# Optimization experiments

Hardware: AMD Instinct MI355X
Metric: run time of the kernel (lower is better)

## Reference

```python
import jax, jax.numpy as jnp
import numpy as np
import math

S, B, F, D, H, L, DFF, PRED = 448, 64, 8, 256, 8, 4, 256, 96
DK = D // H
EPS = 1e-5


def _pos_enc(length, d_model):
    pos = jnp.arange(length, dtype=jnp.float32)[:, None]            # [S,1]
    div = jnp.exp(jnp.arange(0, d_model, 2, dtype=jnp.float32) * (-math.log(10000.0) / d_model))
    pe = jnp.zeros((length, d_model), jnp.float32)
    pe = pe.at[:, 0::2].set(jnp.sin(pos * div))
    pe = pe.at[:, 1::2].set(jnp.cos(pos * div))
    return pe[:, None, :]                                            # [S,1,D]


def _layernorm(x, g, b):
    mu = jnp.mean(x, axis=-1, keepdims=True)
    var = jnp.mean((x - mu) ** 2, axis=-1, keepdims=True)
    return (x - mu) / jnp.sqrt(var + EPS) * g + b


def setup_inputs() -> dict:
    key = jax.random.key(0)
    ks = jax.random.split(key, 12)
    g = lambda k, shape: (jax.random.normal(k, shape) * 0.02).astype(jnp.float32)
    return {
        "src": jax.random.normal(ks[0], (S, B, F), jnp.float32),
        "w_in": g(ks[1], (F, D)), "b_in": jnp.zeros((D,), jnp.float32),
        "Wq": g(ks[2], (L, D, D)), "bq": jnp.zeros((L, D), jnp.float32),
        "Wk": g(ks[3], (L, D, D)), "bk": jnp.zeros((L, D), jnp.float32),
        "Wv": g(ks[4], (L, D, D)), "bv": jnp.zeros((L, D), jnp.float32),
        "Wo": g(ks[5], (L, D, D)), "bo": jnp.zeros((L, D), jnp.float32),
        "g1": jnp.ones((L, D), jnp.float32), "be1": jnp.zeros((L, D), jnp.float32),
        "W1": g(ks[6], (L, D, DFF)), "b1": jnp.zeros((L, DFF), jnp.float32),
        "W2": g(ks[7], (L, DFF, D)), "b2": jnp.zeros((L, D), jnp.float32),
        "g2": jnp.ones((L, D), jnp.float32), "be2": jnp.zeros((L, D), jnp.float32),
        "w_out": g(ks[8], (D, F)), "b_out": jnp.zeros((F,), jnp.float32),
    }


def reference(src, w_in, b_in, Wq, bq, Wk, bk, Wv, bv, Wo, bo,
              g1, be1, W1, b1, W2, b2, g2, be2, w_out, b_out):
    x = src @ w_in + b_in                 # [S,B,D]
    x = x + _pos_enc(S, D)

    scale = math.sqrt(DK)

    def layer(x, p):
        wq, bq_, wk, bk_, wv, bv_, wo, bo_, g1_, be1_, w1, b1_, w2, b2_, g2_, be2_ = p
        Q = (x @ wq + bq_).reshape(S, B, H, DK)
        K = (x @ wk + bk_).reshape(S, B, H, DK)
        V = (x @ wv + bv_).reshape(S, B, H, DK)
        scores = jnp.einsum("sbhd,tbhd->bhst", Q, K) / scale   # [B,H,S,S]
        attn = jax.nn.softmax(scores, axis=-1)
        ctx = jnp.einsum("bhst,tbhd->sbhd", attn, V).reshape(S, B, D)
        x = _layernorm(x + (ctx @ wo + bo_), g1_, be1_)
        ff = jax.nn.relu(x @ w1 + b1_) @ w2 + b2_
        x = _layernorm(x + ff, g2_, be2_)
        return x, None

    x, _ = jax.lax.scan(layer, x, (Wq, bq, Wk, bk, Wv, bv, Wo, bo,
                                   g1, be1, W1, b1, W2, b2, g2, be2))
    return x[-PRED:] @ w_out + b_out      # [PRED,B,F]
```

## Files before the change

### kernel.cpp

```cpp
#include <hip/hip_runtime.h>
#include <hip/hip_bf16.h>
#include <math.h>

#define S_ 448
#define B_ 64
#define F_ 8
#define D_ 256
#define H_ 8
#define DK_ 32
#define L_ 4
#define PRED_ 96
#define NT_ (S_ * B_)
#define PANEL_ (S_ * DK_)
#define VTP_ (32 * 512)
#define SCQ_ 0.25503484f

typedef unsigned short bf16_t;
using bf16x8 = __attribute__((ext_vector_type(8))) short;
using f32x4  = __attribute__((ext_vector_type(4))) float;
using f32x16 = __attribute__((ext_vector_type(16))) float;

__device__ __forceinline__ float b2f(bf16_t b) {
  return __uint_as_float(((unsigned)b) << 16);
}
__device__ __forceinline__ bf16_t f2b(float f) {
  unsigned u = __float_as_uint(f);
  u += 0x7fffu + ((u >> 16) & 1u);
  return (bf16_t)(u >> 16);
}
__device__ __forceinline__ unsigned pk2(float lo, float hi) {
  union { __hip_bfloat162 h; unsigned u; } c;
  c.h = __float22bfloat162_rn(make_float2(lo, hi));
  return c.u;
}
__device__ __forceinline__ void gload16(const bf16_t* g, char* l) {
  __builtin_amdgcn_global_load_lds(
      (const __attribute__((address_space(1))) unsigned*)g,
      (__attribute__((address_space(3))) unsigned*)l, 16, 0, 0);
}

__global__ __launch_bounds__(256) void embed_kernel(
    const float* __restrict__ src, const float* __restrict__ w_in,
    const float* __restrict__ b_in, bf16_t* __restrict__ x) {
  int n = blockIdx.x;
  int d = threadIdx.x;
  const float* srow = src + (size_t)n * F_;
  float acc = b_in[d];
#pragma unroll
  for (int f = 0; f < F_; ++f) acc += srow[f] * w_in[f * D_ + d];
  int s = n / B_;
  int i2 = d & ~1;
  float freq = __expf(-9.210340371976184f * (float)i2 / (float)D_);
  float ang = (float)s * freq;
  float pe = (d & 1) ? cosf(ang) : sinf(ang);
  x[(size_t)n * D_ + d] = f2b(acc + pe);
}

__global__ __launch_bounds__(256) void transpose_w_kernel(
    const float* __restrict__ W, bf16_t* __restrict__ Wt, float scale) {
  __shared__ float t[32][33];
  int l = blockIdx.z;
  int k0 = blockIdx.x * 32, n0 = blockIdx.y * 32;
  int x = threadIdx.x, y = threadIdx.y;
  const float* src = W + ((size_t)l * 256 + k0) * 256 + n0;
#pragma unroll
  for (int i = y; i < 32; i += 8) t[i][x] = src[(size_t)i * 256 + x];
  __syncthreads();
  bf16_t* dst = Wt + ((size_t)l * 256 + n0) * 256 + k0;
#pragma unroll
  for (int i = y; i < 32; i += 8) dst[(size_t)i * 256 + x] = f2b(t[x][i] * scale);
}

__global__ __launch_bounds__(512) void vtrans_kernel(
    const bf16_t* __restrict__ V, bf16_t* __restrict__ Vt) {
  __shared__ bf16_t t[32][456];
  int bh = blockIdx.x, tid = threadIdx.x;
  const bf16_t* Vp = V + (size_t)bh * PANEL_;
#pragma unroll
  for (int p = 0; p < 4; ++p) {
    int idx = tid + p * 512;
    if (idx < 1792) {
      int s = idx >> 2, c = idx & 3;
      uint4 v = *(const uint4*)(Vp + s * 32 + c * 8);
      unsigned w[4] = {v.x, v.y, v.z, v.w};
#pragma unroll
      for (int e = 0; e < 8; ++e) {
        bf16_t val = (bf16_t)((e & 1) ? (w[e >> 1] >> 16) : (w[e >> 1] & 0xffff));
        *(bf16_t*)((char*)&t[0][0] + (c * 8 + e) * 912 + s * 2) = val;
      }
    }
  }
  __syncthreads();
  bf16_t* Op = Vt + (size_t)bh * VTP_;
#pragma unroll
  for (int p = 0; p < 4; ++p) {
    int idx = tid + p * 512;
    int dk = idx >> 6, sl = idx & 63;
    uint4 v = {0, 0, 0, 0};
    if (sl < 56) v = *(const uint4*)((char*)&t[0][0] + dk * 912 + sl * 16);
    *(uint4*)(Op + dk * 512 + sl * 8) = v;
  }
}

template <int ALAY, int OLAY, int RELU>
__device__ __forceinline__ void gemm_body(
    const bf16_t* __restrict__ A, const bf16_t* __restrict__ Wt,
    const float* __restrict__ bias, float bscale, bf16_t* __restrict__ Y,
    int m0, int n0) {
  __shared__ bf16_t As[2][128][32];
  __shared__ bf16_t Bs[2][128][32];
  int tid = threadIdx.x, lane = tid & 63, wv = tid >> 6;
  int wr = wv >> 2, wc = wv & 3;
  int jg = lane >> 4, fr = lane & 15;
  int s_row = tid >> 2;
  int s_p = tid & 3;

  auto stage = [&](int kt, int buf) {
    int k0 = kt * 32;
    int ls = s_p ^ ((s_row >> 1) & 3);
    const bf16_t* ap;
    if (ALAY == 0) {
      ap = A + (size_t)(m0 + s_row) * 256 + k0 + ls * 8;
    } else {
      int n = m0 + s_row;
      int k = k0 + ls * 8;
      ap = A + ((size_t)(((n & 63) << 3) | (k >> 5)) * S_ + (n >> 6)) * DK_ +
           (k & 31);
    }
    const bf16_t* bp = Wt + (size_t)(n0 + s_row) * 256 + k0 + ls * 8;
    gload16(ap, (char*)As + buf * 8192 + wv * 1024);
    gload16(bp, (char*)Bs + buf * 8192 + wv * 1024);
  };

  f32x4 zero = {0.f, 0.f, 0.f, 0.f};
  f32x4 acc[4][2];
#pragma unroll
  for (int i = 0; i < 4; ++i)
#pragma unroll
    for (int j = 0; j < 2; ++j) acc[i][j] = zero;

  stage(0, 0);
  __syncthreads();

  for (int kt = 0; kt < 8; ++kt) {
    int buf = kt & 1;
    if (kt < 7) stage(kt + 1, buf ^ 1);
    bf16x8 af[4], bfr[2];
#pragma unroll
    for (int mi = 0; mi < 4; ++mi) {
      int row = wr * 64 + mi * 16 + fr;
      af[mi] = *(const bf16x8*)((const char*)&As[buf][0][0] + row * 64 +
                                ((jg ^ ((row >> 1) & 3)) << 4));
    }
#pragma unroll
    for (int ni = 0; ni < 2; ++ni) {
      int rn = wc * 32 + ni * 16 + fr;
      bfr[ni] = *(const bf16x8*)((const char*)&Bs[buf][0][0] + rn * 64 +
                                 ((jg ^ ((rn >> 1) & 3)) << 4));
    }
#pragma unroll
    for (int mi = 0; mi < 4; ++mi)
#pragma unroll
      for (int ni = 0; ni < 2; ++ni)
        acc[mi][ni] = __builtin_amdgcn_mfma_f32_16x16x32_bf16(
            af[mi], bfr[ni], acc[mi][ni], 0, 0, 0);
    __syncthreads();
  }

  char* ep0 = (char*)&As[0][0][0] + wv * 1024;
  float bcol[2];
#pragma unroll
  for (int ni = 0; ni < 2; ++ni)
    bcol[ni] = bias[n0 + wc * 32 + ni * 16 + fr] * bscale;
#pragma unroll
  for (int mi = 0; mi < 4; ++mi) {
    char* ep = ep0 + (mi & 1) * 8192;
#pragma unroll
    for (int ni = 0; ni < 2; ++ni)
#pragma unroll
      for (int r = 0; r < 4; ++r) {
        float v = acc[mi][ni][r] + bcol[ni];
        if (RELU) v = fmaxf(v, 0.f);
        int row = jg * 4 + r;
        int cb = (ni * 16 + fr) * 2;
        *(bf16_t*)(ep + row * 64 + (cb ^ (jg << 4))) = f2b(v);
      }
    int row16 = lane >> 2, c = lane & 3;
    uint4 v = *(uint4*)(ep + row16 * 64 +
                        ((c << 4) ^ (((row16 >> 2) & 3) << 4)));
    int n = m0 + wr * 64 + mi * 16 + row16;
    if (OLAY == 0) {
      *(uint4*)((char*)(Y + (size_t)n * 256 + n0 + wc * 32) + c * 16) = v;
    } else {
      int h = (n0 + wc * 32) >> 5;
      *(uint4*)((char*)(Y + ((size_t)(((n & 63) << 3) | h) * S_ + (n >> 6)) *
                                DK_) +
                c * 16) = v;
    }
  }
}

template <int OLAY>
__device__ __forceinline__ void gemm_wide_body(
    const bf16_t* __restrict__ A, const bf16_t* __restrict__ Wt,
    const float* __restrict__ bias, float bscale, bf16_t* __restrict__ Y,
    int m0) {
  __shared__ char smem[49152];
  int tid = threadIdx.x, lane = tid & 63, wv = tid >> 6;
  int wr = wv >> 2, wc = wv & 3;
  int jg = lane >> 4, fr = lane & 15;

  auto stage = [&](int kt, int buf) {
    int k0 = kt * 32;
    int row = tid >> 2, p = tid & 3;
    int ls = p ^ ((row >> 1) & 3);
    gload16(A + (size_t)(m0 + row) * 256 + k0 + ls * 8,
            smem + buf * 8192 + wv * 1024);
    int r1 = 128 + row;
    gload16(Wt + (size_t)row * 256 + k0 + ls * 8,
            smem + 16384 + buf * 16384 + wv * 1024);
    gload16(Wt + (size_t)r1 * 256 + k0 + (p ^ ((r1 >> 1) & 3)) * 8,
            smem + 16384 + buf * 16384 + 8192 + wv * 1024);
  };

  f32x4 zero = {0.f, 0.f, 0.f, 0.f};
  f32x4 acc[4][4];
#pragma unroll
  for (int i = 0; i < 4; ++i)
#pragma unroll
    for (int j = 0; j < 4; ++j) acc[i][j] = zero;

  stage(0, 0);
  __syncthreads();

  for (int kt = 0; kt < 8; ++kt) {
    int buf = kt & 1;
    if (kt < 7) stage(kt + 1, buf ^ 1);
    bf16x8 af[4], bfr[4];
#pragma unroll
    for (int mi = 0; mi < 4; ++mi) {
      int row = wr * 64 + mi * 16 + fr;
      af[mi] = *(const bf16x8*)(smem + buf * 8192 + row * 64 +
                                ((jg ^ ((row >> 1) & 3)) << 4));
    }
#pragma unroll
    for (int ni = 0; ni < 4; ++ni) {
      int rn = wc * 64 + ni * 16 + fr;
      bfr[ni] = *(const bf16x8*)(smem + 16384 + buf * 16384 + rn * 64 +
                                 ((jg ^ ((rn >> 1) & 3)) << 4));
    }
#pragma unroll
    for (int mi = 0; mi < 4; ++mi)
#pragma unroll
      for (int ni = 0; ni < 4; ++ni)
        acc[mi][ni] = __builtin_amdgcn_mfma_f32_16x16x32_bf16(
            af[mi], bfr[ni], acc[mi][ni], 0, 0, 0);
    __syncthreads();
  }

  float bcol[4];
#pragma unroll
  for (int ni = 0; ni < 4; ++ni)
    bcol[ni] = bias[wc * 64 + ni * 16 + fr] * bscale;
#pragma unroll
  for (int mi = 0; mi < 4; ++mi) {
    char* ep = smem + ((mi & 1) ? 16384 : 0) + wv * 2048;
#pragma unroll
    for (int ni = 0; ni < 4; ++ni)
#pragma unroll
      for (int r = 0; r < 4; ++r) {
        float v = acc[mi][ni][r] + bcol[ni];
        int row = jg * 4 + r;
        int cb = (ni * 16 + fr) * 2;
        *(bf16_t*)(ep + row * 128 + (cb ^ (jg << 4))) = f2b(v);
      }
    int row16 = lane >> 2;
    int n = m0 + wr * 64 + mi * 16 + row16;
#pragma unroll
    for (int ps = 0; ps < 2; ++ps) {
      int ch = (lane & 3) + ps * 4;
      uint4 v = *(uint4*)(ep + row16 * 128 +
                          ((ch * 16) ^ (((row16 >> 2) & 3) << 4)));
      if (OLAY == 0) {
        *(uint4*)((char*)(Y + (size_t)n * 256 + wc * 64) + ch * 16) = v;
      } else {
        int h = wc * 2 + (ch >> 2);
        *(uint4*)((char*)(Y + ((size_t)(((n & 63) << 3) | h) * S_ +
                               (n >> 6)) * DK_) +
                  (ch & 3) * 16) = v;
      }
    }
  }
}

__global__ __launch_bounds__(512, 2) void gemm_qkv_kernel(
    const bf16_t* __restrict__ A, const bf16_t* __restrict__ wq,
    const bf16_t* __restrict__ wk, const bf16_t* __restrict__ wvp,
    const float* __restrict__ bq, const float* __restrict__ bk,
    const float* __restrict__ bvp, bf16_t* __restrict__ yq,
    bf16_t* __restrict__ yk, bf16_t* __restrict__ yv) {
  int bid = blockIdx.x;
  int w = (bid & 7) * 84 + (bid >> 3);
  int mtx = w % 3;
  int m0 = (w / 3) * 128;
  const bf16_t* W = mtx == 0 ? wq : mtx == 1 ? wk : wvp;
  const float* bb = mtx == 0 ? bq : mtx == 1 ? bk : bvp;
  bf16_t* Y = mtx == 0 ? yq : mtx == 1 ? yk : yv;
  float bscale = mtx == 0 ? SCQ_ : 1.0f;
  gemm_wide_body<1>(A, W, bb, bscale, Y, m0);
}

__global__ __launch_bounds__(512, 4) void gemm_relu_kernel(
    const bf16_t* __restrict__ A, const bf16_t* __restrict__ Wt,
    const float* __restrict__ bias, bf16_t* __restrict__ Y) {
  int bid = blockIdx.x;
  int w = (bid & 7) * 56 + (bid >> 3);
  gemm_body<0, 0, 1>(A, Wt, bias, 1.0f, Y, (w >> 1) * 128, (w & 1) * 128);
}

template <int ALAY>
__global__ __launch_bounds__(512, 2) void gemm_ln_kernel(
    const bf16_t* __restrict__ A, const bf16_t* __restrict__ Wt,
    const float* __restrict__ bias, const float* __restrict__ g,
    const float* __restrict__ be, bf16_t* __restrict__ x) {
  __shared__ char smem[40960];
  int tid = threadIdx.x, lane = tid & 63, wv = tid >> 6;
  int wr = wv >> 2, wc = wv & 3;
  int jg = lane >> 4, fr = lane & 15;
  int bid = blockIdx.x;
  int m0 = ((bid & 7) * 56 + (bid >> 3)) * 64;

  auto stage = [&](int kt, int buf) {
    int k0 = kt * 32;
    if (tid < 256) {
      int row = tid >> 2, p = tid & 3;
      int ls = p ^ ((row >> 1) & 3);
      const bf16_t* ap;
      if (ALAY == 0) {
        ap = A + (size_t)(m0 + row) * 256 + k0 + ls * 8;
      } else {
        int n = m0 + row;
        int k = k0 + ls * 8;
        ap = A + ((size_t)(((n & 63) << 3) | (k >> 5)) * S_ + (n >> 6)) * DK_ +
             (k & 31);
      }
      gload16(ap, smem + buf * 4096 + wv * 1024);
    }
    int p = tid & 3;
    int r0 = tid >> 2, r1 = 128 + (tid >> 2);
    gload16(Wt + (size_t)r0 * 256 + k0 + (p ^ ((r0 >> 1) & 3)) * 8,
            smem + 8192 + buf * 16384 + wv * 1024);
    gload16(Wt + (size_t)r1 * 256 + k0 + (p ^ ((r1 >> 1) & 3)) * 8,
            smem + 8192 + buf * 16384 + 8192 + wv * 1024);
  };

  f32x4 zero = {0.f, 0.f, 0.f, 0.f};
  f32x4 acc[2][4];
#pragma unroll
  for (int i = 0; i < 2; ++i)
#pragma unroll
    for (int j = 0; j < 4; ++j) acc[i][j] = zero;

  stage(0, 0);
  __syncthreads();

  for (int kt = 0; kt < 8; ++kt) {
    int buf = kt & 1;
    if (kt < 7) stage(kt + 1, buf ^ 1);
    bf16x8 af[2], bfr[4];
#pragma unroll
    for (int mi = 0; mi < 2; ++mi) {
      int row = wr * 32 + mi * 16 + fr;
      af[mi] = *(const bf16x8*)(smem + buf * 4096 + row * 64 +
                                ((jg ^ ((row >> 1) & 3)) << 4));
    }
#pragma unroll
    for (int ni = 0; ni < 4; ++ni) {
      int rn = wc * 64 + ni * 16 + fr;
      bfr[ni] = *(const bf16x8*)(smem + 8192 + buf * 16384 + rn * 64 +
                                 ((jg ^ ((rn >> 1) & 3)) << 4));
    }
#pragma unroll
    for (int mi = 0; mi < 2; ++mi)
#pragma unroll
      for (int ni = 0; ni < 4; ++ni)
        acc[mi][ni] = __builtin_amdgcn_mfma_f32_16x16x32_bf16(
            af[mi], bfr[ni], acc[mi][ni], 0, 0, 0);
    __syncthreads();
  }

  float* ssum = (float*)smem;
  float* ssq  = (float*)(smem + 1024);
  float* rowm = (float*)(smem + 2048);
  float* rowr = (float*)(smem + 2304);

  float bcol[4], gv[4], bev[4];
#pragma unroll
  for (int ni = 0; ni < 4; ++ni) {
    int c = wc * 64 + ni * 16 + fr;
    bcol[ni] = bias[c];
    gv[ni] = g[c];
    bev[ni] = be[c];
  }
#pragma unroll
  for (int mi = 0; mi < 2; ++mi)
#pragma unroll
    for (int r = 0; r < 4; ++r) {
      int row = wr * 32 + mi * 16 + jg * 4 + r;
      size_t gbase = (size_t)(m0 + row) * 256 + wc * 64 + fr;
      float s = 0.f, s2 = 0.f;
#pragma unroll
      for (int ni = 0; ni < 4; ++ni) {
        float v = acc[mi][ni][r] + bcol[ni] + b2f(x[gbase + ni * 16]);
        acc[mi][ni][r] = v;
        s += v;
        s2 += v * v;
      }
#pragma unroll
      for (int off = 1; off <= 8; off <<= 1) {
        s += __shfl_xor(s, off);
        s2 += __shfl_xor(s2, off);
      }
      if (fr == 0) {
        ssum[row * 4 + wc] = s;
        ssq[row * 4 + wc] = s2;
      }
    }
  __syncthreads();
  if (tid < 64) {
    float s = ssum[tid * 4] + ssum[tid * 4 + 1] + ssum[tid * 4 + 2] +
              ssum[tid * 4 + 3];
    float q = ssq[tid * 4] + ssq[tid * 4 + 1] + ssq[tid * 4 + 2] +
              ssq[tid * 4 + 3];
    float mean = s * (1.f / 256.f);
    float var = q * (1.f / 256.f) - mean * mean;
    rowm[tid] = mean;
    rowr[tid] = rsqrtf(var + 1e-5f);
  }
  __syncthreads();
  char* ep0 = smem + 8192 + wv * 2048;
#pragma unroll
  for (int mi = 0; mi < 2; ++mi) {
    char* ep = ep0 + mi * 16384;
#pragma unroll
    for (int r = 0; r < 4; ++r) {
      int row = wr * 32 + mi * 16 + jg * 4 + r;
      float mean = rowm[row], rinv = rowr[row];
#pragma unroll
      for (int ni = 0; ni < 4; ++ni) {
        float lnv = (acc[mi][ni][r] - mean) * rinv * gv[ni] + bev[ni];
        int cb = (ni * 16 + fr) * 2;
        *(bf16_t*)(ep + (jg * 4 + r) * 128 + (cb ^ (jg << 4))) = f2b(lnv);
      }
    }
    int row16 = lane >> 2;
#pragma unroll
    for (int ps = 0; ps < 2; ++ps) {
      int ch = (lane & 3) + ps * 4;
      uint4 v = *(uint4*)(ep + row16 * 128 + ((ch * 16) ^ ((row16 >> 2) << 4)));
      *(uint4*)(x + (size_t)(m0 + wr * 32 + mi * 16 + row16) * 256 + wc * 64 +
                ch * 8) = v;
    }
  }
}

__global__ __launch_bounds__(448) void attn_v8_kernel(
    bf16_t* __restrict__ Q, const bf16_t* __restrict__ K,
    const bf16_t* __restrict__ Vt) {
  __shared__ char Ep[7][2560];
  int tid = threadIdx.x, lane = tid & 63, wv = tid >> 6;
  int bid = blockIdx.x;
  int xcd = bid & 7, j = bid >> 3;
  int bh = ((j >> 1) << 3) | xcd;
  int half = j & 1;
  int q0 = (half * 7 + wv) * 32;
  bf16_t* Qp = Q + (size_t)bh * PANEL_;
  const bf16_t* Kp = K + (size_t)bh * PANEL_;
  const bf16_t* Vp = Vt + (size_t)bh * VTP_;
  int lo31 = lane & 31, hi = lane >> 5;
  const f32x16 z16 = {0.f, 0.f, 0.f, 0.f, 0.f, 0.f, 0.f, 0.f,
                      0.f, 0.f, 0.f, 0.f, 0.f, 0.f, 0.f, 0.f};

  bf16x8 qf0 = *(const bf16x8*)(Qp + (q0 + lo31) * 32 + hi * 8);
  bf16x8 qf1 = *(const bf16x8*)(Qp + (q0 + lo31) * 32 + 16 + hi * 8);

  const bf16_t* kr = Kp + lo31 * 32 + hi * 8;
  const bf16_t* vr = Vp + lo31 * 512 + hi * 8;

  float m_run = -3.0e38f, l_run = 0.f;
  f32x16 o = z16;

#define CHUNK(K0, K1, V0, V1)                                                 \
  {                                                                           \
    f32x16 s = z16;                                                           \
    __builtin_amdgcn_s_setprio(1);                                            \
    s = __builtin_amdgcn_mfma_f32_32x32x16_bf16(K0, qf0, s, 0, 0, 0);         \
    s = __builtin_amdgcn_mfma_f32_32x32x16_bf16(K1, qf1, s, 0, 0, 0);         \
    __builtin_amdgcn_s_setprio(0);                                            \
                                             \
    float x0 = fmaxf(s[0], s[1]), x1 = fmaxf(s[2], s[3]);                     \
    float x2 = fmaxf(s[4], s[5]), x3 = fmaxf(s[6], s[7]);                     \
    float x4 = fmaxf(s[8], s[9]), x5 = fmaxf(s[10], s[11]);                   \
    float x6 = fmaxf(s[12], s[13]), x7 = fmaxf(s[14], s[15]);                 \
    float y0 = fmaxf(x0, x1), y1 = fmaxf(x2, x3);                             \
    float y2 = fmaxf(x4, x5), y3 = fmaxf(x6, x7);                             \
    float cm = fmaxf(fmaxf(y0, y1), fmaxf(y2, y3));                           \
    cm = fmaxf(cm, __shfl_xor(cm, 32));                                       \
    if (!__all(cm <= m_run + 8.0f)) {                                         \
      float mn = fmaxf(m_run, cm);                                            \
      float sc = exp2f(m_run - mn);                                           \
      l_run *= sc;                                                            \
      _Pragma("unroll") for (int r = 0; r < 16; ++r) o[r] *= sc;              \
      m_run = mn;                                                             \
    }                                                                         \
    _Pragma("unroll") for (int r = 0; r < 16; ++r) s[r] = exp2f(s[r] - m_run);\
                                             \
    float u0 = s[0] + s[1], u1 = s[2] + s[3];                                 \
    float u2 = s[4] + s[5], u3 = s[6] + s[7];                                 \
    float u4 = s[8] + s[9], u5 = s[10] + s[11];                               \
    float u6 = s[12] + s[13], u7 = s[14] + s[15];                             \
    float w0 = u0 + u1, w1 = u2 + u3, w2 = u4 + u5, w3 = u6 + u7;             \
    float ls = (w0 + w1) + (w2 + w3);                                         \
    ls += __shfl_xor(ls, 32);                                                 \
    l_run += ls;                                                              \
    {                                                                         \
      unsigned a0 = pk2(s[0], s[1]), a1 = pk2(s[2], s[3]);                    \
      unsigned b0 = pk2(s[4], s[5]), b1 = pk2(s[6], s[7]);                    \
      unsigned xa0 = (unsigned)__shfl_xor((int)a0, 32);                       \
      unsigned xa1 = (unsigned)__shfl_xor((int)a1, 32);                       \
      unsigned xb0 = (unsigned)__shfl_xor((int)b0, 32);                       \
      unsigned xb1 = (unsigned)__shfl_xor((int)b1, 32);                       \
      union { unsigned u[4]; bf16x8 v; } pf;                                  \
      pf.u[0] = hi ? xb0 : a0;                                                \
      pf.u[1] = hi ? xb1 : a1;                                                \
      pf.u[2] = hi ? b0 : xa0;                                                \
      pf.u[3] = hi ? b1 : xa1;                                                \
      o = __builtin_amdgcn_mfma_f32_32x32x16_bf16(pf.v, V0, o, 0, 0, 0);      \
    }                                                                         \
    {                                                                         \
      unsigned a0 = pk2(s[8], s[9]), a1 = pk2(s[10], s[11]);                  \
      unsigned b0 = pk2(s[12], s[13]), b1 = pk2(s[14], s[15]);                \
      unsigned xa0 = (unsigned)__shfl_xor((int)a0, 32);                       \
      unsigned xa1 = (unsigned)__shfl_xor((int)a1, 32);                       \
      unsigned xb0 = (unsigned)__shfl_xor((int)b0, 32);                       \
      unsigned xb1 = (unsigned)__shfl_xor((int)b1, 32);                       \
      union { unsigned u[4]; bf16x8 v; } pf;                                  \
      pf.u[0] = hi ? xb0 : a0;                                                \
      pf.u[1] = hi ? xb1 : a1;                                                \
      pf.u[2] = hi ? b0 : xa0;                                                \
      pf.u[3] = hi ? b1 : xa1;                                                \
      o = __builtin_amdgcn_mfma_f32_32x32x16_bf16(pf.v, V1, o, 0, 0, 0);      \
    }                                                                         \
  }

  bf16x8 ck0 = *(const bf16x8*)(kr);
  bf16x8 ck1 = *(const bf16x8*)(kr + 16);
  bf16x8 cv0 = *(const bf16x8*)(vr);
  bf16x8 cv1 = *(const bf16x8*)(vr + 16);

  for (int kc = 0; kc < 14; kc += 2) {
    const bf16_t* krn = kr + (kc + 1) * 1024;
    const bf16_t* vrn = vr + (kc + 1) * 32;
    bf16x8 nk0 = *(const bf16x8*)(krn);
    bf16x8 nk1 = *(const bf16x8*)(krn + 16);
    bf16x8 nv0 = *(const bf16x8*)(vrn);
    bf16x8 nv1 = *(const bf16x8*)(vrn + 16);
    CHUNK(ck0, ck1, cv0, cv1)
    if (kc + 2 < 14) {
      const bf16_t* krm = kr + (kc + 2) * 1024;
      const bf16_t* vrm = vr + (kc + 2) * 32;
      ck0 = *(const bf16x8*)(krm);
      ck1 = *(const bf16x8*)(krm + 16);
      cv0 = *(const bf16x8*)(vrm);
      cv1 = *(const bf16x8*)(vrm + 16);
    }
    CHUNK(nk0, nk1, nv0, nv1)
  }
#undef CHUNK

  float inv = 1.f / l_run;
  char* ep = &Ep[wv][0];
#pragma unroll
  for (int r = 0; r < 16; ++r) {
    int q = (r & 3) + 8 * (r >> 2) + 4 * hi;
    float iq = __shfl(inv, q);
    *(bf16_t*)(ep + q * 80 + lo31 * 2) = f2b(o[r] * iq);
  }
#pragma unroll
  for (int ps = 0; ps < 2; ++ps) {
    int row = ps * 16 + (lane >> 2), ch = lane & 3;
    uint4 v = *(uint4*)(ep + row * 80 + ch * 16);
    *(uint4*)(Qp + (q0 + row) * 32 + ch * 8) = v;
  }
}

__global__ __launch_bounds__(512) void attn_v3f_kernel(
    bf16_t* __restrict__ Q, const bf16_t* __restrict__ K,
    const bf16_t* __restrict__ Vsrc) {
  __shared__ bf16_t Vt[32][520];
  __shared__ char Pbuf[8][2048];
  int tid = threadIdx.x, lane = tid & 63, wv = tid >> 6;
  int bid = blockIdx.x;
  int bh = (bid & 7) | ((bid >> 5) << 3);
  int chunk = (bid >> 3) & 3;
  bf16_t* Qp = Q + (size_t)bh * PANEL_;
  const bf16_t* Kp = K + (size_t)bh * PANEL_;
  int jg = lane >> 4, fr = lane & 15;

  const bf16_t* Vp = Vsrc + (size_t)bh * PANEL_;
  for (int idx = tid; idx < 448 * 4; idx += 512) {
    int t = idx >> 2, c = idx & 3;
    uint4 vv = *(const uint4*)(Vp + t * 32 + c * 8);
    unsigned w[4] = {vv.x, vv.y, vv.z, vv.w};
#pragma unroll
    for (int e = 0; e < 8; ++e) {
      bf16_t val = (bf16_t)((e & 1) ? (w[e >> 1] >> 16) : (w[e >> 1] & 0xffff));
      *(bf16_t*)((char*)&Vt[0][0] + (c * 8 + e) * 1040 + t * 2) = val;
    }
  }
  __syncthreads();

  int q0 = chunk * 128 + wv * 16;
  if (q0 < S_) {
    f32x4 zero = {0.f, 0.f, 0.f, 0.f};
    bf16x8 qf = *(const bf16x8*)(Qp + (q0 + fr) * 32 + jg * 8);
    f32x4 s2[28];
#pragma unroll
    for (int ct = 0; ct < 28; ++ct) {
      bf16x8 kf = *(const bf16x8*)(Kp + (ct * 16 + fr) * 32 + jg * 8);
      s2[ct] = __builtin_amdgcn_mfma_f32_16x16x32_bf16(kf, qf, zero, 0, 0, 0);
    }
    float m = s2[0][0];
#pragma unroll
    for (int ct = 0; ct < 28; ++ct)
#pragma unroll
      for (int r = 0; r < 4; ++r) m = fmaxf(m, s2[ct][r]);
    m = fmaxf(m, __shfl_xor(m, 16));
    m = fmaxf(m, __shfl_xor(m, 32));
    float l = 0.f;
#pragma unroll
    for (int ct = 0; ct < 28; ++ct)
#pragma unroll
      for (int r = 0; r < 4; ++r) {
        float p = exp2f(s2[ct][r] - m);
        s2[ct][r] = p;
        l += p;
      }
    l += __shfl_xor(l, 16);
    l += __shfl_xor(l, 32);
    float inv = 1.f / l;

    char* pb0 = &Pbuf[wv][0];
    f32x4 o[2] = {zero, zero};
#pragma unroll
    for (int c = 0; c < 14; ++c) {
      char* pb = pb0 + (c & 1) * 1024;
      uint2 w0, w1;
      w0.x = pk2(s2[2 * c][0], s2[2 * c][1]);
      w0.y = pk2(s2[2 * c][2], s2[2 * c][3]);
      w1.x = pk2(s2[2 * c + 1][0], s2[2 * c + 1][1]);
      w1.y = pk2(s2[2 * c + 1][2], s2[2 * c + 1][3]);
      *(uint2*)(pb + fr * 64 + 8 * jg) = w0;
      *(uint2*)(pb + fr * 64 + 32 + 8 * jg) = w1;
      bf16x8 pf = *(const bf16x8*)(pb + fr * 64 + jg * 16);
#pragma unroll
      for (int nt = 0; nt < 2; ++nt) {
        bf16x8 vf = *(const bf16x8*)((const char*)&Vt[0][0] +
                                     (nt * 16 + fr) * 1040 +
                                     (c * 32 + jg * 8) * 2);
        o[nt] = __builtin_amdgcn_mfma_f32_16x16x32_bf16(pf, vf, o[nt], 0, 0, 0);
      }
    }
    float invq[4];
#pragma unroll
    for (int r = 0; r < 4; ++r) invq[r] = __shfl(inv, jg * 4 + r);
#pragma unroll
    for (int nt = 0; nt < 2; ++nt)
#pragma unroll
      for (int r = 0; r < 4; ++r) {
        float v = o[nt][r] * invq[r];
        int row = jg * 4 + r;
        int cb = (nt * 16 + fr) * 2;
        *(bf16_t*)(pb0 + row * 64 + (cb ^ (jg << 4))) = f2b(v);
      }
    {
      int row16 = lane >> 2, c = lane & 3;
      uint4 v = *(uint4*)(pb0 + row16 * 64 +
                          ((c << 4) ^ (((row16 >> 2) & 3) << 4)));
      *(uint4*)(Qp + (q0 + row16) * 32 + c * 8) = v;
    }
  }
}

__global__ __launch_bounds__(256) void out_kernel(
    const bf16_t* __restrict__ x, const float* __restrict__ w_out,
    const float* __restrict__ b_out, float* __restrict__ out) {
  int idx = blockIdx.x * 256 + threadIdx.x;
  int f = idx & 7;
  int pb = idx >> 3;
  const bf16_t* xrow = x + ((size_t)(S_ - PRED_) * B_ + pb) * D_;
  float acc = b_out[f];
  for (int dd = 0; dd < D_; ++dd) acc += b2f(xrow[dd]) * w_out[dd * F_ + f];
  out[idx] = acc;
}

extern "C" void kernel_launch(void* const* d_in, const int* in_sizes, int n_in,
                              void* d_out, int out_size, void* d_ws, size_t ws_size,
                              hipStream_t stream) {
  const float* src  = (const float*)d_in[0];
  const float* w_in = (const float*)d_in[1];
  const float* b_in = (const float*)d_in[2];
  const float* Wq = (const float*)d_in[3];
  const float* bq = (const float*)d_in[4];
  const float* Wk = (const float*)d_in[5];
  const float* bk = (const float*)d_in[6];
  const float* Wv = (const float*)d_in[7];
  const float* bv = (const float*)d_in[8];
  const float* Wo = (const float*)d_in[9];
  const float* bo = (const float*)d_in[10];
  const float* g1 = (const float*)d_in[11];
  const float* be1 = (const float*)d_in[12];
  const float* W1 = (const float*)d_in[13];
  const float* b1 = (const float*)d_in[14];
  const float* W2 = (const float*)d_in[15];
  const float* b2 = (const float*)d_in[16];
  const float* g2 = (const float*)d_in[17];
  const float* be2 = (const float*)d_in[18];
  const float* w_out = (const float*)d_in[19];
  const float* b_out = (const float*)d_in[20];
  float* out = (float*)d_out;

  const size_t NTD = (size_t)NT_ * D_;
  bf16_t* xb = (bf16_t*)d_ws;
  bf16_t* qb = xb + NTD;
  bf16_t* kb = qb + NTD;
  bf16_t* vb = kb + NTD;
  bf16_t* wt = vb + NTD;
  const size_t WSZ = (size_t)L_ * 65536;
  bf16_t* wtq = wt;
  bf16_t* wtk = wtq + WSZ;
  bf16_t* wtv = wtk + WSZ;
  bf16_t* wto = wtv + WSZ;
  bf16_t* wt1 = wto + WSZ;
  bf16_t* wt2 = wt1 + WSZ;
  bf16_t* vtb = wt2 + WSZ;

  const size_t NEED = ((size_t)4 * NTD + 6 * WSZ + (size_t)512 * VTP_) * 2;
  const int use_vt = (ws_size >= NEED) ? 1 : 0;

  dim3 tb(32, 8), tg(8, 8, L_);
  transpose_w_kernel<<<tg, tb, 0, stream>>>(Wq, wtq, SCQ_);
  transpose_w_kernel<<<tg, tb, 0, stream>>>(Wk, wtk, 1.0f);
  transpose_w_kernel<<<tg, tb, 0, stream>>>(Wv, wtv, 1.0f);
  transpose_w_kernel<<<tg, tb, 0, stream>>>(Wo, wto, 1.0f);
  transpose_w_kernel<<<tg, tb, 0, stream>>>(W1, wt1, 1.0f);
  transpose_w_kernel<<<tg, tb, 0, stream>>>(W2, wt2, 1.0f);

  embed_kernel<<<NT_, 256, 0, stream>>>(src, w_in, b_in, xb);

  for (int l = 0; l < L_; ++l) {
    const size_t woff = (size_t)l * 65536;
    const size_t boff = (size_t)l * D_;
    gemm_qkv_kernel<<<672, 512, 0, stream>>>(
        xb, wtq + woff, wtk + woff, wtv + woff, bq + boff, bk + boff,
        bv + boff, qb, kb, vb);
    if (use_vt) {
      vtrans_kernel<<<512, 512, 0, stream>>>(vb, vtb);
      attn_v8_kernel<<<1024, 448, 0, stream>>>(qb, kb, vtb);
    } else {
      attn_v3f_kernel<<<2048, 512, 0, stream>>>(qb, kb, vb);
    }
    gemm_ln_kernel<1><<<448, 512, 0, stream>>>(qb, wto + woff, bo + boff,
                                               g1 + boff, be1 + boff, xb);
    gemm_relu_kernel<<<448, 512, 0, stream>>>(xb, wt1 + woff, b1 + boff, qb);
    gemm_ln_kernel<0><<<448, 512, 0, stream>>>(qb, wt2 + woff, b2 + boff,
                                               g2 + boff, be2 + boff, xb);
  }

  out_kernel<<<(PRED_ * B_ * F_) / 256, 256, 0, stream>>>(xb, w_out, b_out, out);
}
```

Baseline: 522.5 us.

## Fuse FFN up-projection, ReLU, down-projection and LayerNorm into one kernel

```diff
diff --git a/kernel.cpp b/kernel.cpp
--- a/kernel.cpp
+++ b/kernel.cpp
@@ -99,104 +99,6 @@
     uint4 v = {0, 0, 0, 0};
     if (sl < 56) v = *(const uint4*)((char*)&t[0][0] + dk * 912 + sl * 16);
     *(uint4*)(Op + dk * 512 + sl * 8) = v;
-  }
-}
-
-template <int ALAY, int OLAY, int RELU>
-__device__ __forceinline__ void gemm_body(
-    const bf16_t* __restrict__ A, const bf16_t* __restrict__ Wt,
-    const float* __restrict__ bias, float bscale, bf16_t* __restrict__ Y,
-    int m0, int n0) {
-  __shared__ bf16_t As[2][128][32];
-  __shared__ bf16_t Bs[2][128][32];
-  int tid = threadIdx.x, lane = tid & 63, wv = tid >> 6;
-  int wr = wv >> 2, wc = wv & 3;
-  int jg = lane >> 4, fr = lane & 15;
-  int s_row = tid >> 2;
-  int s_p = tid & 3;
-
-  auto stage = [&](int kt, int buf) {
-    int k0 = kt * 32;
-    int ls = s_p ^ ((s_row >> 1) & 3);
-    const bf16_t* ap;
-    if (ALAY == 0) {
-      ap = A + (size_t)(m0 + s_row) * 256 + k0 + ls * 8;
-    } else {
-      int n = m0 + s_row;
-      int k = k0 + ls * 8;
-      ap = A + ((size_t)(((n & 63) << 3) | (k >> 5)) * S_ + (n >> 6)) * DK_ +
-           (k & 31);
-    }
-    const bf16_t* bp = Wt + (size_t)(n0 + s_row) * 256 + k0 + ls * 8;
-    gload16(ap, (char*)As + buf * 8192 + wv * 1024);
-    gload16(bp, (char*)Bs + buf * 8192 + wv * 1024);
-  };
-
-  f32x4 zero = {0.f, 0.f, 0.f, 0.f};
-  f32x4 acc[4][2];
-#pragma unroll
-  for (int i = 0; i < 4; ++i)
-#pragma unroll
-    for (int j = 0; j < 2; ++j) acc[i][j] = zero;
-
-  stage(0, 0);
-  __syncthreads();
-
-  for (int kt = 0; kt < 8; ++kt) {
-    int buf = kt & 1;
-    if (kt < 7) stage(kt + 1, buf ^ 1);
-    bf16x8 af[4], bfr[2];
-#pragma unroll
-    for (int mi = 0; mi < 4; ++mi) {
-      int row = wr * 64 + mi * 16 + fr;
-      af[mi] = *(const bf16x8*)((const char*)&As[buf][0][0] + row * 64 +
-                                ((jg ^ ((row >> 1) & 3)) << 4));
-    }
-#pragma unroll
-    for (int ni = 0; ni < 2; ++ni) {
-      int rn = wc * 32 + ni * 16 + fr;
-      bfr[ni] = *(const bf16x8*)((const char*)&Bs[buf][0][0] + rn * 64 +
-                                 ((jg ^ ((rn >> 1) & 3)) << 4));
-    }
-#pragma unroll
-    for (int mi = 0; mi < 4; ++mi)
-#pragma unroll
-      for (int ni = 0; ni < 2; ++ni)
-        acc[mi][ni] = __builtin_amdgcn_mfma_f32_16x16x32_bf16(
-            af[mi], bfr[ni], acc[mi][ni], 0, 0, 0);
-    __syncthreads();
-  }
-
-  char* ep0 = (char*)&As[0][0][0] + wv * 1024;
-  float bcol[2];
-#pragma unroll
-  for (int ni = 0; ni < 2; ++ni)
-    bcol[ni] = bias[n0 + wc * 32 + ni * 16 + fr] * bscale;
-#pragma unroll
-  for (int mi = 0; mi < 4; ++mi) {
-    char* ep = ep0 + (mi & 1) * 8192;
-#pragma unroll
-    for (int ni = 0; ni < 2; ++ni)
-#pragma unroll
-      for (int r = 0; r < 4; ++r) {
-        float v = acc[mi][ni][r] + bcol[ni];
-        if (RELU) v = fmaxf(v, 0.f);
-        int row = jg * 4 + r;
-        int cb = (ni * 16 + fr) * 2;
-        *(bf16_t*)(ep + row * 64 + (cb ^ (jg << 4))) = f2b(v);
-      }
-    int row16 = lane >> 2, c = lane & 3;
-    uint4 v = *(uint4*)(ep + row16 * 64 +
-                        ((c << 4) ^ (((row16 >> 2) & 3) << 4)));
-    int n = m0 + wr * 64 + mi * 16 + row16;
-    if (OLAY == 0) {
-      *(uint4*)((char*)(Y + (size_t)n * 256 + n0 + wc * 32) + c * 16) = v;
-    } else {
-      int h = (n0 + wc * 32) >> 5;
-      *(uint4*)((char*)(Y + ((size_t)(((n & 63) << 3) | h) * S_ + (n >> 6)) *
-                                DK_) +
-                c * 16) = v;
-    }
   }
 }
 
@@ -310,14 +212,6 @@
   gemm_wide_body<1>(A, W, bb, bscale, Y, m0);
 }
 
-__global__ __launch_bounds__(512, 4) void gemm_relu_kernel(
-    const bf16_t* __restrict__ A, const bf16_t* __restrict__ Wt,
-    const float* __restrict__ bias, bf16_t* __restrict__ Y) {
-  int bid = blockIdx.x;
-  int w = (bid & 7) * 56 + (bid >> 3);
-  gemm_body<0, 0, 1>(A, Wt, bias, 1.0f, Y, (w >> 1) * 128, (w & 1) * 128);
-}
-
 template <int ALAY>
 __global__ __launch_bounds__(512, 2) void gemm_ln_kernel(
     const bf16_t* __restrict__ A, const bf16_t* __restrict__ Wt,
@@ -449,6 +343,199 @@
 #pragma unroll
       for (int ni = 0; ni < 4; ++ni) {
         float lnv = (acc[mi][ni][r] - mean) * rinv * gv[ni] + bev[ni];
+        int cb = (ni * 16 + fr) * 2;
+        *(bf16_t*)(ep + (jg * 4 + r) * 128 + (cb ^ (jg << 4))) = f2b(lnv);
+      }
+    }
+    int row16 = lane >> 2;
+#pragma unroll
+    for (int ps = 0; ps < 2; ++ps) {
+      int ch = (lane & 3) + ps * 4;
+      uint4 v = *(uint4*)(ep + row16 * 128 + ((ch * 16) ^ ((row16 >> 2) << 4)));
+      *(uint4*)(x + (size_t)(m0 + wr * 32 + mi * 16 + row16) * 256 + wc * 64 +
+                ch * 8) = v;
+    }
+  }
+}
+
+__global__ __launch_bounds__(512, 2) void gemm_ffn_kernel(
+    const bf16_t* __restrict__ Wt1, const float* __restrict__ b1v,
+    const bf16_t* __restrict__ Wt2, const float* __restrict__ b2v,
+    const float* __restrict__ g, const float* __restrict__ be,
+    bf16_t* __restrict__ x) {
+  __shared__ char smem[65536];
+  int tid = threadIdx.x, lane = tid & 63, wv = tid >> 6;
+  int wr = wv >> 2, wc = wv & 3;
+  int jg = lane >> 4, fr = lane & 15;
+  int bid = blockIdx.x;
+  int m0 = ((bid & 7) * 56 + (bid >> 3)) * 64;
+
+  auto stageA = [&](int kt, int buf) {
+    if (tid < 256) {
+      int row = tid >> 2, p = tid & 3;
+      int ls = p ^ ((row >> 1) & 3);
+      gload16(x + (size_t)(m0 + row) * 256 + kt * 32 + ls * 8,
+              smem + buf * 4096 + wv * 1024);
+    }
+  };
+  auto stageB = [&](const bf16_t* W, int kt, int buf) {
+    int p = tid & 3;
+    int r0 = tid >> 2, r1 = 128 + (tid >> 2);
+    gload16(W + (size_t)r0 * 256 + kt * 32 + (p ^ ((r0 >> 1) & 3)) * 8,
+            smem + 32768 + buf * 16384 + wv * 1024);
+    gload16(W + (size_t)r1 * 256 + kt * 32 + (p ^ ((r1 >> 1) & 3)) * 8,
+            smem + 32768 + buf * 16384 + 8192 + wv * 1024);
+  };
+
+  f32x4 zero = {0.f, 0.f, 0.f, 0.f};
+  f32x4 acc[2][4];
+#pragma unroll
+  for (int i = 0; i < 2; ++i)
+#pragma unroll
+    for (int j = 0; j < 4; ++j) acc[i][j] = zero;
+
+  stageA(0, 0);
+  stageB(Wt1, 0, 0);
+  __syncthreads();
+  for (int kt = 0; kt < 8; ++kt) {
+    int buf = kt & 1;
+    if (kt < 7) { stageA(kt + 1, buf ^ 1); stageB(Wt1, kt + 1, buf ^ 1); }
+    bf16x8 af[2], bfr[4];
+#pragma unroll
+    for (int mi = 0; mi < 2; ++mi) {
+      int row = wr * 32 + mi * 16 + fr;
+      af[mi] = *(const bf16x8*)(smem + buf * 4096 + row * 64 +
+                                ((jg ^ ((row >> 1) & 3)) << 4));
+    }
+#pragma unroll
+    for (int ni = 0; ni < 4; ++ni) {
+      int rn = wc * 64 + ni * 16 + fr;
+      bfr[ni] = *(const bf16x8*)(smem + 32768 + buf * 16384 + rn * 64 +
+                                 ((jg ^ ((rn >> 1) & 3)) << 4));
+    }
+#pragma unroll
+    for (int mi = 0; mi < 2; ++mi)
+#pragma unroll
+      for (int ni = 0; ni < 4; ++ni)
+        acc[mi][ni] = __builtin_amdgcn_mfma_f32_16x16x32_bf16(
+            af[mi], bfr[ni], acc[mi][ni], 0, 0, 0);
+    __syncthreads();
+  }
+
+  stageB(Wt2, 0, 0);
+
+  {
+    float b1c[4];
+#pragma unroll
+    for (int ni = 0; ni < 4; ++ni) b1c[ni] = b1v[wc * 64 + ni * 16 + fr];
+#pragma unroll
+    for (int mi = 0; mi < 2; ++mi)
+#pragma unroll
+      for (int ni = 0; ni < 4; ++ni)
+#pragma unroll
+        for (int r = 0; r < 4; ++r) {
+          float v = fmaxf(acc[mi][ni][r] + b1c[ni], 0.f);
+          int row = wr * 32 + mi * 16 + jg * 4 + r;
+          int col = wc * 64 + ni * 16 + fr;
+          int kt2 = col >> 5, c = col & 31;
+          *(bf16_t*)(smem + kt2 * 4096 + row * 64 +
+                     (((c >> 3) ^ ((row >> 1) & 3)) << 4) + (c & 7) * 2) =
+              f2b(v);
+        }
+  }
+  __syncthreads();
+
+  f32x4 acc2[2][4];
+#pragma unroll
+  for (int i = 0; i < 2; ++i)
+#pragma unroll
+    for (int j = 0; j < 4; ++j) acc2[i][j] = zero;
+
+  for (int kt = 0; kt < 8; ++kt) {
+    int buf = kt & 1;
+    if (kt < 7) stageB(Wt2, kt + 1, buf ^ 1);
+    bf16x8 af[2], bfr[4];
+#pragma unroll
+    for (int mi = 0; mi < 2; ++mi) {
+      int row = wr * 32 + mi * 16 + fr;
+      af[mi] = *(const bf16x8*)(smem + kt * 4096 + row * 64 +
+                                ((jg ^ ((row >> 1) & 3)) << 4));
+    }
+#pragma unroll
+    for (int ni = 0; ni < 4; ++ni) {
+      int rn = wc * 64 + ni * 16 + fr;
+      bfr[ni] = *(const bf16x8*)(smem + 32768 + buf * 16384 + rn * 64 +
+                                 ((jg ^ ((rn >> 1) & 3)) << 4));
+    }
+#pragma unroll
+    for (int mi = 0; mi < 2; ++mi)
+#pragma unroll
+      for (int ni = 0; ni < 4; ++ni)
+        acc2[mi][ni] = __builtin_amdgcn_mfma_f32_16x16x32_bf16(
+            af[mi], bfr[ni], acc2[mi][ni], 0, 0, 0);
+    __syncthreads();
+  }
+
+  float* ssum = (float*)smem;
+  float* ssq  = (float*)(smem + 1024);
+  float* rowm = (float*)(smem + 2048);
+  float* rowr = (float*)(smem + 2304);
+
+  float bcol[4], gv[4], bev[4];
+#pragma unroll
+  for (int ni = 0; ni < 4; ++ni) {
+    int c = wc * 64 + ni * 16 + fr;
+    bcol[ni] = b2v[c];
+    gv[ni] = g[c];
+    bev[ni] = be[c];
+  }
+#pragma unroll
+  for (int mi = 0; mi < 2; ++mi)
+#pragma unroll
+    for (int r = 0; r < 4; ++r) {
+      int row = wr * 32 + mi * 16 + jg * 4 + r;
+      size_t gbase = (size_t)(m0 + row) * 256 + wc * 64 + fr;
+      float s = 0.f, s2 = 0.f;
+#pragma unroll
+      for (int ni = 0; ni < 4; ++ni) {
+        float v = acc2[mi][ni][r] + bcol[ni] + b2f(x[gbase + ni * 16]);
+        acc2[mi][ni][r] = v;
+        s += v;
+        s2 += v * v;
+      }
+#pragma unroll
+      for (int off = 1; off <= 8; off <<= 1) {
+        s += __shfl_xor(s, off);
+        s2 += __shfl_xor(s2, off);
+      }
+      if (fr == 0) {
+        ssum[row * 4 + wc] = s;
+        ssq[row * 4 + wc] = s2;
+      }
+    }
+  __syncthreads();
+  if (tid < 64) {
+    float s = ssum[tid * 4] + ssum[tid * 4 + 1] + ssum[tid * 4 + 2] +
+              ssum[tid * 4 + 3];
+    float q = ssq[tid * 4] + ssq[tid * 4 + 1] + ssq[tid * 4 + 2] +
+              ssq[tid * 4 + 3];
+    float mean = s * (1.f / 256.f);
+    float var = q * (1.f / 256.f) - mean * mean;
+    rowm[tid] = mean;
+    rowr[tid] = rsqrtf(var + 1e-5f);
+  }
+  __syncthreads();
+  char* ep0 = smem + 32768 + wv * 2048;
+#pragma unroll
+  for (int mi = 0; mi < 2; ++mi) {
+    char* ep = ep0 + mi * 16384;
+#pragma unroll
+    for (int r = 0; r < 4; ++r) {
+      int row = wr * 32 + mi * 16 + jg * 4 + r;
+      float mean = rowm[row], rinv = rowr[row];
+#pragma unroll
+      for (int ni = 0; ni < 4; ++ni) {
+        float lnv = (acc2[mi][ni][r] - mean) * rinv * gv[ni] + bev[ni];
         int cb = (ni * 16 + fr) * 2;
         *(bf16_t*)(ep + (jg * 4 + r) * 128 + (cb ^ (jg << 4))) = f2b(lnv);
       }
@@ -692,6 +779,40 @@
   }
 }
 
+__global__ __launch_bounds__(256) void resid_ln_fallback_kernel(
+    bf16_t* __restrict__ x, const bf16_t* __restrict__ y,
+    const float* __restrict__ g, const float* __restrict__ be) {
+  int wv = threadIdx.x >> 6, lane = threadIdx.x & 63;
+  size_t n = (size_t)blockIdx.x * 4 + wv;
+  size_t off = n * D_ + lane * 4;
+  ushort4 xv = *(const ushort4*)(x + off);
+  ushort4 yv = *(const ushort4*)(y + off);
+  float v[4];
+  v[0] = b2f(xv.x) + b2f(yv.x);
+  v[1] = b2f(xv.y) + b2f(yv.y);
+  v[2] = b2f(xv.z) + b2f(yv.z);
+  v[3] = b2f(xv.w) + b2f(yv.w);
+  float sm = v[0] + v[1] + v[2] + v[3];
+#pragma unroll
+  for (int o = 32; o; o >>= 1) sm += __shfl_xor(sm, o);
+  float mean = sm * (1.f / 256.f);
+  float c[4], s2 = 0.f;
+#pragma unroll
+  for (int i = 0; i < 4; ++i) { c[i] = v[i] - mean; s2 += c[i] * c[i]; }
+#pragma unroll
+  for (int o = 32; o; o >>= 1) s2 += __shfl_xor(s2, o);
+  float var = s2 * (1.f / 256.f);
+  float r = rsqrtf(var + 1e-5f);
+  float4 gv = *(const float4*)(g + lane * 4);
+  float4 bv = *(const float4*)(be + lane * 4);
+  ushort4 ov;
+  ov.x = f2b(c[0] * r * gv.x + bv.x);
+  ov.y = f2b(c[1] * r * gv.y + bv.y);
+  ov.z = f2b(c[2] * r * gv.z + bv.z);
+  ov.w = f2b(c[3] * r * gv.w + bv.w);
+  *(ushort4*)(x + off) = ov;
+}
+
 __global__ __launch_bounds__(256) void out_kernel(
     const bf16_t* __restrict__ x, const float* __restrict__ w_out,
     const float* __restrict__ b_out, float* __restrict__ out) {
@@ -772,9 +893,9 @@
     }
     gemm_ln_kernel<1><<<448, 512, 0, stream>>>(qb, wto + woff, bo + boff,
                                                g1 + boff, be1 + boff, xb);
-    gemm_relu_kernel<<<448, 512, 0, stream>>>(xb, wt1 + woff, b1 + boff, qb);
-    gemm_ln_kernel<0><<<448, 512, 0, stream>>>(qb, wt2 + woff, b2 + boff,
-                                               g2 + boff, be2 + boff, xb);
+    gemm_ffn_kernel<<<448, 512, 0, stream>>>(wt1 + woff, b1 + boff,
+                                             wt2 + woff, b2 + boff,
+                                             g2 + boff, be2 + boff, xb);
   }
 
   out_kernel<<<(PRED_ * B_ * F_) / 256, 256, 0, stream>>>(xb, w_out, b_out, out);
```

Result: faster. 487.2 us (-6.8%).
